# Kernel optimization log

Measured on AMD Instinct MI355X. Metric: run time of the kernel, lower is better.

The kernel has to match this reference:

```python
import jax, jax.numpy as jnp
import numpy as np

Tx, V, D = 512, 100, 64
DM, NH, DFF, NL = 512, 8, 2048, 2
H, DATT, FCH, OUT = 256, 128, 256, 2


def setup_inputs() -> dict:
    key = jax.random.key(0)
    ks = jax.random.split(key, 16)
    s = 0.02
    w = lambda k, shape: jax.random.normal(k, shape, jnp.float32) * s
    return dict(
        x_data=jax.random.normal(ks[0], (1, Tx, V, D), jnp.float32),
        feat_w=w(ks[1], (DM, D)), feat_b=jnp.zeros((DM,), jnp.float32),
        in_w=w(ks[2], (NL, 3 * DM, DM)), in_b=jnp.zeros((NL, 3 * DM), jnp.float32),
        out_w=w(ks[3], (NL, DM, DM)), out_b=jnp.zeros((NL, DM), jnp.float32),
        ff1_w=w(ks[4], (NL, DFF, DM)), ff1_b=jnp.zeros((NL, DFF), jnp.float32),
        ff2_w=w(ks[5], (NL, DM, DFF)), ff2_b=jnp.zeros((NL, DM), jnp.float32),
        ln1_g=jnp.ones((NL, DM), jnp.float32), ln1_b=jnp.zeros((NL, DM), jnp.float32),
        ln2_g=jnp.ones((NL, DM), jnp.float32), ln2_b=jnp.zeros((NL, DM), jnp.float32),
        att1_w=w(ks[6], (DATT, DM + H)), att1_b=jnp.zeros((DATT,), jnp.float32),
        att2_w=w(ks[7], (1, DATT)), att2_b=jnp.zeros((1,), jnp.float32),
        lstm_wih=w(ks[8], (4 * H, DM)), lstm_whh=w(ks[9], (4 * H, H)),
        lstm_bih=jnp.zeros((4 * H,), jnp.float32), lstm_bhh=jnp.zeros((4 * H,), jnp.float32),
        fc1_w=w(ks[10], (FCH, DM + H)), fc1_b=jnp.zeros((FCH,), jnp.float32),
        fc2_w=w(ks[11], (OUT, FCH)), fc2_b=jnp.zeros((OUT,), jnp.float32),
    )


def _layernorm(x, g, b):
    m = x.mean(-1, keepdims=True)
    v = x.var(-1, keepdims=True)
    return (x - m) * jax.lax.rsqrt(v + 1e-5) * g + b


def _forward(x_data, feat_w, feat_b, in_w, in_b, out_w, out_b, ff1_w, ff1_b,
             ff2_w, ff2_b, ln1_g, ln1_b, ln2_g, ln2_b, att1_w, att1_b,
             att2_w, att2_b, lstm_wih, lstm_whh, lstm_bih, lstm_bhh,
             fc1_w, fc1_b, fc2_w, fc2_b):
    x = x_data[0]                              # [Tx, V, D]
    x = jnp.swapaxes(x, 0, 1)                  # [V, Tx, D]  (seq=V, batch=Tx)
    x = x @ feat_w.T + feat_b                  # feature mapping -> [V, Tx, DM]
    # sinusoidal positional encoding over the V (seq) axis
    pos = jnp.arange(V, dtype=jnp.float32)[:, None]
    div = jnp.exp(jnp.arange(0, DM, 2, dtype=jnp.float32) * (-np.log(10000.0) / DM))
    pe = jnp.zeros((V, DM), jnp.float32)
    pe = pe.at[:, 0::2].set(jnp.sin(pos * div)).at[:, 1::2].set(jnp.cos(pos * div))
    x = x + pe[:, None, :]
    hd = DM // NH
    for l in range(NL):                        # post-norm TransformerEncoderLayer
        qkv = x @ in_w[l].T + in_b[l]          # [V, Tx, 3*DM]
        q, k, v = jnp.split(qkv, 3, axis=-1)
        q = q.reshape(V, Tx, NH, hd)
        k = k.reshape(V, Tx, NH, hd)
        v = v.reshape(V, Tx, NH, hd)
        scores = jnp.einsum('ibhd,jbhd->bhij', q, k) / np.sqrt(hd).astype(np.float32)
        attn = jax.nn.softmax(scores, axis=-1)
        ctx = jnp.einsum('bhij,jbhd->ibhd', attn, v).reshape(V, Tx, DM)
        x = _layernorm(x + ctx @ out_w[l].T + out_b[l], ln1_g[l], ln1_b[l])
        ff = jax.nn.relu(x @ ff1_w[l].T + ff1_b[l]) @ ff2_w[l].T + ff2_b[l]
        x = _layernorm(x + ff, ln2_g[l], ln2_b[l])
    hs = jnp.swapaxes(x, 0, 1)                 # [Tx, V, DM]

    def step(carry, h_i):                      # h_i: [V, DM]
        s_h, s_c = carry                       # [1, H] each
        att_in = jnp.concatenate([h_i, jnp.broadcast_to(s_h, (V, H))], axis=1)
        a1 = jnp.tanh(att_in @ att1_w.T + att1_b)
        a2 = a1 @ att2_w.T + att2_b            # [V, 1]
        a2 = a2 - jnp.max(a2)
        alpha = jnp.exp(a2)
        alpha = alpha / (jnp.sum(alpha, axis=0, keepdims=True) + 1e-15)
        c = jnp.sum(alpha * h_i, axis=0, keepdims=True)   # [1, DM]
        gates = c @ lstm_wih.T + lstm_bih + s_h @ lstm_whh.T + lstm_bhh
        i_g, f_g, g_g, o_g = jnp.split(gates, 4, axis=-1)
        s_c_new = jax.nn.sigmoid(f_g) * s_c + jax.nn.sigmoid(i_g) * jnp.tanh(g_g)
        s_h_new = jax.nn.sigmoid(o_g) * jnp.tanh(s_c_new)
        fc_in = jnp.concatenate([c, s_h], axis=1)  # uses PREVIOUS hidden, per original
        fc = jax.nn.relu(fc_in @ fc1_w.T + fc1_b) @ fc2_w.T + fc2_b
        log_prob = jax.nn.log_softmax(fc, axis=1)  # [1, OUT]
        return (s_h_new, s_c_new), log_prob

    init = (jnp.zeros((1, H), jnp.float32), jnp.zeros((1, H), jnp.float32))
    _, logs = jax.lax.scan(step, init, hs)
    return logs[-1]                            # last timestep's log-probs [1, OUT]


def reference(x_data, feat_w, feat_b, in_w, in_b, out_w, out_b, ff1_w, ff1_b,
              ff2_w, ff2_b, ln1_g, ln1_b, ln2_g, ln2_b, att1_w, att1_b,
              att2_w, att2_b, lstm_wih, lstm_whh, lstm_bih, lstm_bhh,
              fc1_w, fc1_b, fc2_w, fc2_b):
    return _forward(x_data, feat_w, feat_b, in_w, in_b, out_w, out_b, ff1_w,
                    ff1_b, ff2_w, ff2_b, ln1_g, ln1_b, ln2_g, ln2_b, att1_w,
                    att1_b, att2_w, att2_b, lstm_wih, lstm_whh, lstm_bih,
                    lstm_bhh, fc1_w, fc1_b, fc2_w, fc2_b)
```

## Files before the change

### kernel.cpp

```cpp
#include <hip/hip_runtime.h>
#include <hip/hip_bf16.h>


typedef __attribute__((ext_vector_type(8))) short short8;
typedef __attribute__((ext_vector_type(4))) float f32x4;

__device__ __forceinline__ int jglob_of(int e0, int jl) { return ((jl >> 4) << 8) + e0 + (jl & 15); }
__device__ __forceinline__ float blo(unsigned u) { return __uint_as_float(u << 16); }
__device__ __forceinline__ float bhi(unsigned u) { return __uint_as_float(u & 0xffff0000u); }
__device__ __forceinline__ short f2bs(float x) {
  union { __hip_bfloat16 h; short s; } u; u.h = __float2bfloat16(x); return u.s;
}
__device__ __forceinline__ float tanhf_fast(float x) {
  float e = __expf(2.f * x);
  return 1.f - 2.f * __builtin_amdgcn_rcpf(e + 1.f);
}

#define GLL16(GSRC, LDST) \
  __builtin_amdgcn_global_load_lds( \
      (const __attribute__((address_space(1))) unsigned int*)(GSRC), \
      (__attribute__((address_space(3))) unsigned int*)(LDST), 16, 0, 0)

__global__ __launch_bounds__(256) void pe_kernel(float* __restrict__ pe) {
  int idx = blockIdx.x * 256 + threadIdx.x;
  if (idx >= 100 * 512) return;
  int v = idx >> 9, n = idx & 511;
  float d = expf(-(float)(n & ~1) * (9.2103403719761836f / 512.0f));
  float ang = (float)v * d;
  pe[idx] = (n & 1) ? cosf(ang) : sinf(ang);
}

__global__ __launch_bounds__(256) void cvt_kernel(const float* __restrict__ src,
                                                  __hip_bfloat16* __restrict__ dst, int n) {
  int i = blockIdx.x * 256 + threadIdx.x;
  if (i < n) dst[i] = __float2bfloat16(src[i]);
}

__global__ __launch_bounds__(256) void gemm_bf16(
    const __hip_bfloat16* __restrict__ A, long aBase, int aDiv, long aSA, long aSB,
    const __hip_bfloat16* __restrict__ W, int ldw,
    const float* __restrict__ bias,
    float* __restrict__ outF, __hip_bfloat16* __restrict__ outB,
    long oBase, int oDiv, long oSA, long oSB,
    int K, int addTo, int relu)
{
  __shared__ __hip_bfloat16 As[128 * 64];
  __shared__ __hip_bfloat16 Bs[128 * 64];
  const int tid = threadIdx.x;
  const int rT = blockIdx.y * 128, nT = blockIdx.x * 128;
  const int wave = tid >> 6, lane = tid & 63;
  const int wr = wave >> 1, wc = wave & 1;
  const int lrow = lane & 15, lkg = lane >> 4;

  long asrc[4], bsrc[4];
  const int sc8 = ((lane & 7) ^ (lane >> 3)) * 8;
#pragma unroll
  for (int i = 0; i < 4; ++i) {
    const int chunk = wave * 4 + i;
    const int row = chunk * 8 + (lane >> 3);
    const int gr = rT + row;
    asrc[i] = aBase + (long)(gr / aDiv) * aSA + (long)(gr % aDiv) * aSB + sc8;
    bsrc[i] = (long)(nT + row) * ldw + sc8;
  }

  f32x4 acc[4][4];
#pragma unroll
  for (int i = 0; i < 4; ++i)
#pragma unroll
    for (int j = 0; j < 4; ++j) acc[i][j] = (f32x4){0.f, 0.f, 0.f, 0.f};

  for (int k0 = 0; k0 < K; k0 += 64) {
#pragma unroll
    for (int i = 0; i < 4; ++i) {
      const int chunk = wave * 4 + i;
      GLL16(A + asrc[i] + k0, &As[chunk * 512]);
      GLL16(W + bsrc[i] + k0, &Bs[chunk * 512]);
    }
    __syncthreads();
#pragma unroll
    for (int ks = 0; ks < 2; ++ks) {
      short8 af[4], bfv[4];
#pragma unroll
      for (int f = 0; f < 4; ++f) {
        const int Ra = wr * 64 + f * 16 + lrow;
        af[f] = *(const short8*)&As[Ra * 64 + (((ks * 4 + lkg) ^ (Ra & 7)) * 8)];
        const int Rb = wc * 64 + f * 16 + lrow;
        bfv[f] = *(const short8*)&Bs[Rb * 64 + (((ks * 4 + lkg) ^ (Rb & 7)) * 8)];
      }
#pragma unroll
      for (int fm = 0; fm < 4; ++fm)
#pragma unroll
        for (int fn = 0; fn < 4; ++fn)
          acc[fm][fn] = __builtin_amdgcn_mfma_f32_16x16x32_bf16(af[fm], bfv[fn], acc[fm][fn], 0, 0, 0);
    }
    __syncthreads();
  }

  float bias_v[4];
#pragma unroll
  for (int fn = 0; fn < 4; ++fn)
    bias_v[fn] = bias ? bias[nT + wc * 64 + fn * 16 + lrow] : 0.f;

#pragma unroll
  for (int fm = 0; fm < 4; ++fm) {
#pragma unroll
    for (int r = 0; r < 4; ++r) {
      const int grow = rT + wr * 64 + fm * 16 + lkg * 4 + r;
      const long obase_r = oBase + (long)(grow / oDiv) * oSA + (long)(grow % oDiv) * oSB;
#pragma unroll
      for (int fn = 0; fn < 4; ++fn) {
        const int gcol = nT + wc * 64 + fn * 16 + lrow;
        float v = acc[fm][fn][r] + bias_v[fn];
        if (relu) v = fmaxf(v, 0.f);
        const long o = obase_r + gcol;
        if (outF) { if (addTo) v += outF[o]; outF[o] = v; }
        else outB[o] = __float2bfloat16(v);
      }
    }
  }
}

__global__ __launch_bounds__(256) void gemm_mfma(
    const float* __restrict__ A, long aBase, int aDiv, long aSA, long aSB,
    const float* __restrict__ W, int ldw,
    const float* __restrict__ bias,
    const float* __restrict__ extra, int extraDiv,
    float* __restrict__ outF, __hip_bfloat16* __restrict__ outB,
    __hip_bfloat16* __restrict__ outB2,
    long oBase, int oDiv, long oSA, long oSB, long oSC,
    int N, int K, int addTo, int relu)
{
  __shared__ short As[2][128][40];
  __shared__ short Bs[2][128][40];
  const int tid = threadIdx.x;
  const int rT = blockIdx.y * 128, nT = blockIdx.x * 128;
  const int wave = tid >> 6, lane = tid & 63;
  const int wr = wave >> 1, wc = wave & 1;
  const int lrow = lane & 15, lkg = lane >> 4;
  const int srow = tid >> 1, shf = tid & 1;

  const long arow = aBase + (long)((rT + srow) / aDiv) * aSA + (long)((rT + srow) % aDiv) * aSB + shf * 16;
  const long brow = (long)(nT + srow) * ldw + shf * 16;

  f32x4 acc[4][4];
#pragma unroll
  for (int i = 0; i < 4; ++i)
#pragma unroll
    for (int j = 0; j < 4; ++j) acc[i][j] = (f32x4){0.f, 0.f, 0.f, 0.f};

  float4 ra[4], rb[4];
#define LOADT(K0) do { \
    const float* _pa = A + arow + (K0); \
    ra[0] = *(const float4*)(_pa); ra[1] = *(const float4*)(_pa + 4); \
    ra[2] = *(const float4*)(_pa + 8); ra[3] = *(const float4*)(_pa + 12); \
    const float* _pb = W + brow + (K0); \
    rb[0] = *(const float4*)(_pb); rb[1] = *(const float4*)(_pb + 4); \
    rb[2] = *(const float4*)(_pb + 8); rb[3] = *(const float4*)(_pb + 12); \
  } while (0)

#define CVST(DST, X, Y) do { \
    short8 _v; \
    _v[0] = f2bs((X).x); _v[1] = f2bs((X).y); _v[2] = f2bs((X).z); _v[3] = f2bs((X).w); \
    _v[4] = f2bs((Y).x); _v[5] = f2bs((Y).y); _v[6] = f2bs((Y).z); _v[7] = f2bs((Y).w); \
    *(short8*)(DST) = _v; \
  } while (0)

#define STAGE(BUF) do { \
    CVST(&As[BUF][srow][shf * 16],     ra[0], ra[1]); \
    CVST(&As[BUF][srow][shf * 16 + 8], ra[2], ra[3]); \
    CVST(&Bs[BUF][srow][shf * 16],     rb[0], rb[1]); \
    CVST(&Bs[BUF][srow][shf * 16 + 8], rb[2], rb[3]); \
  } while (0)

  LOADT(0);
  STAGE(0);
  __syncthreads();

  int cur = 0;
  for (int k0 = 0; k0 < K; k0 += 32) {
    const bool nlast = (k0 + 32 < K);
    if (nlast) LOADT(k0 + 32);
    short8 af[4], bfv[4];
#pragma unroll
    for (int f = 0; f < 4; ++f)
      af[f] = *(const short8*)&As[cur][wr * 64 + f * 16 + lrow][lkg * 8];
#pragma unroll
    for (int f = 0; f < 4; ++f)
      bfv[f] = *(const short8*)&Bs[cur][wc * 64 + f * 16 + lrow][lkg * 8];
#pragma unroll
    for (int fm = 0; fm < 4; ++fm)
#pragma unroll
      for (int fn = 0; fn < 4; ++fn)
        acc[fm][fn] = __builtin_amdgcn_mfma_f32_16x16x32_bf16(af[fm], bfv[fn], acc[fm][fn], 0, 0, 0);
    if (nlast) STAGE(cur ^ 1);
    __syncthreads();
    cur ^= 1;
  }

  float bias_v[4];
#pragma unroll
  for (int fn = 0; fn < 4; ++fn)
    bias_v[fn] = bias ? bias[nT + wc * 64 + fn * 16 + lrow] : 0.f;

#pragma unroll
  for (int fm = 0; fm < 4; ++fm) {
#pragma unroll
    for (int r = 0; r < 4; ++r) {
      const int grow = rT + wr * 64 + fm * 16 + lkg * 4 + r;
      const long obase_r = oBase + (long)(grow / oDiv) * oSA + (long)(grow % oDiv) * oSB;
      const long exrow = (long)(grow / extraDiv) * N;
#pragma unroll
      for (int fn = 0; fn < 4; ++fn) {
        const int gcol = nT + wc * 64 + fn * 16 + lrow;
        float v = acc[fm][fn][r] + bias_v[fn];
        if (extra) v += extra[exrow + gcol];
        if (relu) v = fmaxf(v, 0.f);
        const long o = obase_r + (long)gcol * oSC;
        if (outF) { if (addTo) v += outF[o]; outF[o] = v; }
        else outB[o] = __float2bfloat16(v);
        if (outB2) outB2[o] = __float2bfloat16(v);
      }
    }
  }
#undef LOADT
#undef CVST
#undef STAGE
}

__global__ __launch_bounds__(256) void attn_kernel(
    const __hip_bfloat16* __restrict__ qkv, __hip_bfloat16* __restrict__ outY)
{
  __shared__ float q_s[100][68];
  __shared__ float k_s[100][68];
  __shared__ float v_s[100][68];
  __shared__ float S_s[100][104];
  __shared__ float rs_s[100];
  const int h = blockIdx.x, bl = blockIdx.y, tid = threadIdx.x;

  for (int idx = tid; idx < 100 * 64; idx += 256) {
    int vv = idx >> 6, d = idx & 63;
    long base = ((long)(vv * 128 + bl)) * 1536 + h * 64 + d;
    q_s[vv][d] = __bfloat162float(qkv[base]);
    k_s[vv][d] = __bfloat162float(qkv[base + 512]);
    v_s[vv][d] = __bfloat162float(qkv[base + 1024]);
  }
  __syncthreads();

  const int ty = tid >> 4, tx = tid & 15;
  for (int i0 = 0; i0 < 128; i0 += 64) {
    for (int j0 = 0; j0 < 128; j0 += 64) {
      float acc[4][4];
#pragma unroll
      for (int r = 0; r < 4; ++r)
#pragma unroll
        for (int c = 0; c < 4; ++c) acc[r][c] = 0.f;
      for (int d = 0; d < 64; d += 4) {
        float4 qv[4], kv[4];
#pragma unroll
        for (int r = 0; r < 4; ++r) {
          int ii = i0 + ty * 4 + r; ii = (ii < 100) ? ii : 99;
          qv[r] = *(const float4*)&q_s[ii][d];
        }
#pragma unroll
        for (int c = 0; c < 4; ++c) {
          int jj = j0 + tx * 4 + c; jj = (jj < 100) ? jj : 99;
          kv[c] = *(const float4*)&k_s[jj][d];
        }
#pragma unroll
        for (int r = 0; r < 4; ++r)
#pragma unroll
          for (int c = 0; c < 4; ++c)
            acc[r][c] += qv[r].x * kv[c].x + qv[r].y * kv[c].y + qv[r].z * kv[c].z + qv[r].w * kv[c].w;
      }
#pragma unroll
      for (int r = 0; r < 4; ++r)
#pragma unroll
        for (int c = 0; c < 4; ++c) {
          int ii = i0 + ty * 4 + r, jj = j0 + tx * 4 + c;
          if (ii < 100 && jj < 100) S_s[ii][jj] = acc[r][c] * 0.125f;
        }
    }
  }
  __syncthreads();
  if (tid < 100) {
    float m = -1e30f;
    for (int j = 0; j < 100; ++j) m = fmaxf(m, S_s[tid][j]);
    float s = 0.f;
    for (int j = 0; j < 100; ++j) { float e = __expf(S_s[tid][j] - m); S_s[tid][j] = e; s += e; }
    rs_s[tid] = 1.f / s;
  }
  __syncthreads();
  for (int i0 = 0; i0 < 128; i0 += 64) {
    float acc[4][4];
#pragma unroll
    for (int r = 0; r < 4; ++r)
#pragma unroll
      for (int c = 0; c < 4; ++c) acc[r][c] = 0.f;
    for (int j = 0; j < 100; ++j) {
      float av[4];
#pragma unroll
      for (int r = 0; r < 4; ++r) {
        int ii = i0 + ty * 4 + r; ii = (ii < 100) ? ii : 99;
        av[r] = S_s[ii][j];
      }
      const float4 vv4 = *(const float4*)&v_s[j][tx * 4];
#pragma unroll
      for (int r = 0; r < 4; ++r) {
        acc[r][0] += av[r] * vv4.x; acc[r][1] += av[r] * vv4.y;
        acc[r][2] += av[r] * vv4.z; acc[r][3] += av[r] * vv4.w;
      }
    }
#pragma unroll
    for (int r = 0; r < 4; ++r) {
      int ii = i0 + ty * 4 + r;
      if (ii < 100) {
        float inv = rs_s[ii];
        __hip_bfloat16* op = outY + ((long)ii * 128 + bl) * 512 + h * 64 + tx * 4;
        op[0] = __float2bfloat16(acc[r][0] * inv);
        op[1] = __float2bfloat16(acc[r][1] * inv);
        op[2] = __float2bfloat16(acc[r][2] * inv);
        op[3] = __float2bfloat16(acc[r][3] * inv);
      }
    }
  }
}

__global__ __launch_bounds__(256) void ln_kernel(float* __restrict__ X,
    __hip_bfloat16* __restrict__ Xb,
    const float* __restrict__ g, const float* __restrict__ b)
{
  const int row = blockIdx.x * 4 + (threadIdx.x >> 6);
  const int lane = threadIdx.x & 63;
  float* x = X + (long)row * 512;
  __hip_bfloat16* xb = Xb + (long)row * 512;
  float v[8]; float s = 0.f, sq = 0.f;
#pragma unroll
  for (int i = 0; i < 8; ++i) { v[i] = x[lane + i * 64]; s += v[i]; sq += v[i] * v[i]; }
#pragma unroll
  for (int off = 32; off; off >>= 1) { s += __shfl_xor(s, off, 64); sq += __shfl_xor(sq, off, 64); }
  const float mean = s * (1.f / 512.f);
  const float var = sq * (1.f / 512.f) - mean * mean;
  const float inv = rsqrtf(var + 1e-5f);
#pragma unroll
  for (int i = 0; i < 8; ++i) {
    int c = lane + i * 64;
    float r = (v[i] - mean) * inv * g[c] + b[c];
    x[c] = r;
    xb[c] = __float2bfloat16(r);
  }
}

__global__ void init_kernel(unsigned long long* sh_units, float* c_g) {
  int t = threadIdx.x;
  sh_units[t] = 0ULL;
  sh_units[256 + t] = 0ULL;
  c_g[t] = 0.f; c_g[256 + t] = 0.f;
}

#define DEC_NB 16

__global__ __launch_bounds__(256, 1) void decoder_kernel(
    const float* __restrict__ X,
    const __hip_bfloat16* __restrict__ Pb,
    const __hip_bfloat16* __restrict__ Gb,
    const float* __restrict__ att1_w, const float* __restrict__ att1_b,
    const float* __restrict__ att2_w,
    const float* __restrict__ whh,
    const float* __restrict__ bih, const float* __restrict__ bhh,
    const float* __restrict__ fc1_w, const float* __restrict__ fc1_b,
    const float* __restrict__ fc2_w, const float* __restrict__ fc2_b,
    unsigned long long* sh_units,
    float* c_g,
    float* __restrict__ out)
{
  if (blockIdx.x & 7) return;
  const int tid = threadIdx.x;
  const int blk = blockIdx.x >> 3;
  const int e0 = blk * 16;

  __shared__ __align__(16) float Whh_s[64][260];
  __shared__ __align__(16) unsigned short W1b_s[128][264];
  __shared__ __align__(16) float s_h_s[256];
  __shared__ float w2_s[128], ub_s[128], bsum_s[64];
  __shared__ float u_s[128], sc_s[16];
  __shared__ float a2_s[104];
  __shared__ float red_s[256];
  __shared__ float gates_s[64];
  __shared__ float red4_s[4];
  __shared__ float fcin_s[768];
  __shared__ float fca_s[256];

  for (int idx = tid; idx < 64 * 256; idx += 256) {
    int jl = idx >> 8, k = idx & 255;
    Whh_s[jl][k] = whh[(long)jglob_of(e0, jl) * 256 + k];
  }
  for (int idx = tid; idx < 128 * 256; idx += 256) {
    int j = idx >> 8, k = idx & 255;
    union { __hip_bfloat16 h; unsigned short u; } cv;
    cv.h = __float2bfloat16(att1_w[(long)j * 768 + 512 + k]);
    W1b_s[j][k] = cv.u;
  }
  if (tid < 128) { w2_s[tid] = att2_w[tid]; ub_s[tid] = att1_b[tid]; }
  if (tid < 64) {
    int jg = jglob_of(e0, tid);
    bsum_s[tid] = bih[jg] + bhh[jg];
  }
  if (tid < 16) sc_s[tid] = 0.f;
  if (tid < 4) a2_s[100 + tid] = 0.f;

  const int pv = tid >> 1, ppart = tid & 1;
  const int pvv = (pv < 100) ? pv : 99;
  const int gjl = tid >> 2, gq = tid & 3;
  const long gRowOff = (long)jglob_of(e0, gjl) * 100 + gq * 26;

  unsigned PCa[32], PCb[32];
  unsigned GCa[13], GCb[13];

#define PREFETCH(T1, PCd, GCd) do { \
    const uint4* _pp = (const uint4*)Pb + ((((long)(T1) * 100 + pvv) * 128 + ppart * 64) >> 3); \
    _Pragma("unroll") \
    for (int _i = 0; _i < 8; ++_i) { \
      uint4 _t = _pp[_i]; \
      (PCd)[4*_i] = _t.x; (PCd)[4*_i+1] = _t.y; (PCd)[4*_i+2] = _t.z; (PCd)[4*_i+3] = _t.w; \
    } \
    const unsigned* _gp = (const unsigned*)(Gb + (long)(T1) * 102400 + gRowOff); \
    _Pragma("unroll") \
    for (int _i = 0; _i < 13; ++_i) (GCd)[_i] = _gp[_i]; \
  } while (0)

#define STEP(T, PCc, GCc, PCn, GCn) do { \
     \
    { \
      unsigned long long* _up = &sh_units[((((T) & 1) ^ 1) << 8) + tid]; \
      unsigned long long _v = __hip_atomic_load(_up, __ATOMIC_RELAXED, __HIP_MEMORY_SCOPE_AGENT); \
      while ((unsigned)(_v >> 32) < (unsigned)(T)) { \
        __builtin_amdgcn_s_sleep(1); \
        _v = __hip_atomic_load(_up, __ATOMIC_RELAXED, __HIP_MEMORY_SCOPE_AGENT); \
      } \
      s_h_s[tid] = __uint_as_float((unsigned)_v); \
    } \
    __syncthreads(); \
     \
    if ((T) + 1 < 512) PREFETCH((T) + 1, PCn, GCn); \
     \
    { const int _j = tid >> 1, _hf = tid & 1; \
      const unsigned short* _wrow = &W1b_s[_j][_hf * 128]; \
      const float* _sh = &s_h_s[_hf * 128]; \
      float _a = 0.f; \
      _Pragma("unroll") \
      for (int _i = 0; _i < 16; ++_i) { \
        uint4 _wv = *(const uint4*)(_wrow + 8 * _i); \
        const float4 _s0 = *(const float4*)(_sh + 8 * _i); \
        const float4 _s1 = *(const float4*)(_sh + 8 * _i + 4); \
        _a += blo(_wv.x) * _s0.x + bhi(_wv.x) * _s0.y + blo(_wv.y) * _s0.z + bhi(_wv.y) * _s0.w \
            + blo(_wv.z) * _s1.x + bhi(_wv.z) * _s1.y + blo(_wv.w) * _s1.z + bhi(_wv.w) * _s1.w; \
      } \
      _a += __shfl_xor(_a, 1, 64); \
      if (_hf == 0) u_s[_j] = _a + ub_s[_j]; \
    } \
    float _hhv; \
    { const float* _wr = &Whh_s[gjl][gq * 64]; \
      const float* _sh = &s_h_s[gq * 64]; \
      float _a = 0.f; \
      _Pragma("unroll") \
      for (int _i = 0; _i < 16; ++_i) { \
        const float4 _w4 = *(const float4*)(_wr + 4 * _i); \
        const float4 _s4 = *(const float4*)(_sh + 4 * _i); \
        _a += _w4.x * _s4.x + _w4.y * _s4.y + _w4.z * _s4.z + _w4.w * _s4.w; \
      } \
      _a += __shfl_xor(_a, 1, 64); \
      _a += __shfl_xor(_a, 2, 64); \
      _hhv = _a; \
    } \
    __syncthreads(); \
     \
    { float _val = 0.f; \
      _Pragma("unroll") \
      for (int _jj = 0; _jj < 64; ++_jj) { \
        unsigned _u = (PCc)[_jj >> 1]; \
        float _pf = (_jj & 1) ? bhi(_u) : blo(_u); \
        int _col = ppart * 64 + _jj; \
        _val += tanhf_fast(_pf + u_s[_col]) * w2_s[_col]; \
      } \
      _val += __shfl_xor(_val, 1, 64); \
      if (ppart == 0 && pv < 100) a2_s[pv] = _val; \
    } \
    __syncthreads(); \
     \
    if (tid < 64) { \
      float _x0 = a2_s[tid]; \
      float _x1 = (tid + 64 < 100) ? a2_s[tid + 64] : -3.0e38f; \
      float _m = fmaxf(_x0, _x1); \
      _Pragma("unroll") \
      for (int _o = 32; _o; _o >>= 1) _m = fmaxf(_m, __shfl_xor(_m, _o, 64)); \
      float _e0 = __expf(_x0 - _m); \
      float _e1 = (tid + 64 < 100) ? __expf(_x1 - _m) : 0.f; \
      float _s = _e0 + _e1; \
      _Pragma("unroll") \
      for (int _o = 32; _o; _o >>= 1) _s += __shfl_xor(_s, _o, 64); \
      const float _inv = 1.f / (_s + 1e-15f); \
      a2_s[tid] = _e0 * _inv; \
      if (tid + 64 < 100) a2_s[tid + 64] = _e1 * _inv; \
    } \
    __syncthreads(); \
     \
    { float _p = 0.f; \
      _Pragma("unroll") \
      for (int _i = 0; _i < 13; ++_i) { \
        unsigned _u = (GCc)[_i]; \
        _p += a2_s[gq * 26 + 2 * _i] * blo(_u); \
        _p += a2_s[gq * 26 + 2 * _i + 1] * bhi(_u); \
      } \
      _p += __shfl_xor(_p, 1, 64); \
      _p += __shfl_xor(_p, 2, 64); \
      if (gq == 0) gates_s[gjl] = _p + _hhv + bsum_s[gjl]; \
    } \
    __syncthreads(); \
     \
    if ((T) < 511) { \
      if (tid < 16) { \
        const float _ig = gates_s[tid], _fg = gates_s[16 + tid]; \
        const float _gg = gates_s[32 + tid], _og = gates_s[48 + tid]; \
        const float _si = 1.f / (1.f + __expf(-_ig)); \
        const float _sf = 1.f / (1.f + __expf(-_fg)); \
        const float _so = 1.f / (1.f + __expf(-_og)); \
        const float _sc = _sf * sc_s[tid] + _si * tanhf(_gg); \
        sc_s[tid] = _sc; \
        const float _sh2 = _so * tanhf(_sc); \
        const unsigned long long _v = \
            ((unsigned long long)(unsigned)((T) + 1) << 32) | (unsigned long long)__float_as_uint(_sh2); \
        __hip_atomic_store(&sh_units[(((T) & 1) << 8) + e0 + tid], _v, \
                           __ATOMIC_RELAXED, __HIP_MEMORY_SCOPE_AGENT); \
      } \
    } else { \
      const int _dl = tid & 31, _vs = tid >> 5; \
      const int _v0 = _vs * 13, _v1 = (_v0 + 13 < 100) ? _v0 + 13 : 100; \
      float _ac = 0.f; \
      for (int _v = _v0; _v < _v1; ++_v) \
        _ac += a2_s[_v] * X[((long)(_v * 512 + 511)) * 512 + blk * 32 + _dl]; \
      red_s[tid] = _ac; \
      __syncthreads(); \
      if (tid < 32) { \
        float _cc = 0.f; \
        _Pragma("unroll") \
        for (int _s = 0; _s < 8; ++_s) _cc += red_s[_s * 32 + tid]; \
        __hip_atomic_store(&c_g[blk * 32 + tid], _cc, __ATOMIC_RELAXED, __HIP_MEMORY_SCOPE_AGENT); \
      } \
      __syncthreads(); \
      if (tid == 0) \
        __hip_atomic_store(&sh_units[256 + e0], 512ULL << 32, \
                           __ATOMIC_RELEASE, __HIP_MEMORY_SCOPE_AGENT); \
    } \
  } while (0)

  PREFETCH(0, PCa, GCa);
  __syncthreads();

  for (int t2 = 0; t2 < 512; t2 += 2) {
    STEP(t2,     PCa, GCa, PCb, GCb);
    STEP(t2 + 1, PCb, GCb, PCa, GCa);
  }

  if (blk == 0) {
    if (tid < DEC_NB) {
      while ((unsigned)(__hip_atomic_load(&sh_units[256 + tid * 16],
                 __ATOMIC_RELAXED, __HIP_MEMORY_SCOPE_AGENT) >> 32) < 512u)
        __builtin_amdgcn_s_sleep(1);
    }
    __builtin_amdgcn_fence(__ATOMIC_ACQUIRE, "agent");
    __syncthreads();
    fcin_s[tid]       = __hip_atomic_load(&c_g[tid],       __ATOMIC_RELAXED, __HIP_MEMORY_SCOPE_AGENT);
    fcin_s[256 + tid] = __hip_atomic_load(&c_g[256 + tid], __ATOMIC_RELAXED, __HIP_MEMORY_SCOPE_AGENT);
    fcin_s[512 + tid] = s_h_s[tid];
    __syncthreads();
    float acc = fc1_b[tid];
    const float* w = fc1_w + (long)tid * 768;
    for (int k = 0; k < 768; ++k) acc += w[k] * fcin_s[k];
    fca_s[tid] = fmaxf(acc, 0.f);
    __syncthreads();
    if (tid < 128) {
      const int r = tid >> 6, k0 = tid & 63;
      float a = 0.f;
#pragma unroll
      for (int s = 0; s < 4; ++s) a += fc2_w[r * 256 + k0 + s * 64] * fca_s[k0 + s * 64];
#pragma unroll
      for (int off = 32; off; off >>= 1) a += __shfl_xor(a, off, 64);
      if (k0 == 0) red4_s[r] = a + fc2_b[r];
    }
    __syncthreads();
    if (tid == 0) {
      const float l0 = red4_s[0], l1 = red4_s[1];
      const float m = fmaxf(l0, l1);
      const float ls = logf(__expf(l0 - m) + __expf(l1 - m));
      out[0] = l0 - m - ls;
      out[1] = l1 - m - ls;
    }
  }
#undef PREFETCH
#undef STEP
}

extern "C" void kernel_launch(void* const* d_in, const int* in_sizes, int n_in,
                              void* d_out, int out_size, void* d_ws, size_t ws_size,
                              hipStream_t stream) {
  const float* x_data  = (const float*)d_in[0];
  const float* feat_w  = (const float*)d_in[1];
  const float* feat_b  = (const float*)d_in[2];
  const float* in_w    = (const float*)d_in[3];
  const float* in_b    = (const float*)d_in[4];
  const float* out_w   = (const float*)d_in[5];
  const float* out_b   = (const float*)d_in[6];
  const float* ff1_w   = (const float*)d_in[7];
  const float* ff1_b   = (const float*)d_in[8];
  const float* ff2_w   = (const float*)d_in[9];
  const float* ff2_b   = (const float*)d_in[10];
  const float* ln1_g   = (const float*)d_in[11];
  const float* ln1_b   = (const float*)d_in[12];
  const float* ln2_g   = (const float*)d_in[13];
  const float* ln2_b   = (const float*)d_in[14];
  const float* att1_w  = (const float*)d_in[15];
  const float* att1_b  = (const float*)d_in[16];
  const float* att2_w  = (const float*)d_in[17];
  const float* lstm_wih = (const float*)d_in[19];
  const float* lstm_whh = (const float*)d_in[20];
  const float* lstm_bih = (const float*)d_in[21];
  const float* lstm_bhh = (const float*)d_in[22];
  const float* fc1_w   = (const float*)d_in[23];
  const float* fc1_b   = (const float*)d_in[24];
  const float* fc2_w   = (const float*)d_in[25];
  const float* fc2_b   = (const float*)d_in[26];

  float* ws   = (float*)d_ws;
  float* Xf   = ws;
  float* R    = Xf + 26214400;
  __hip_bfloat16* Xb   = (__hip_bfloat16*)R;
  __hip_bfloat16* qkvb = (__hip_bfloat16*)(R + 13107200);
  __hip_bfloat16* ctxb = (__hip_bfloat16*)(R + 22937600);
  __hip_bfloat16* ffh  = (__hip_bfloat16*)(R + 13107200);
  __hip_bfloat16* wb   = (__hip_bfloat16*)(R + 26214400);
  __hip_bfloat16* in_wb  = wb;
  __hip_bfloat16* out_wb = wb + 1572864;
  __hip_bfloat16* ff1_wb = out_wb + 524288;
  __hip_bfloat16* ff2_wb = ff1_wb + 2097152;
  __hip_bfloat16* PbB = (__hip_bfloat16*)R;
  __hip_bfloat16* GbB = (__hip_bfloat16*)(R + 3276800);
  float* pe    = R + 29491200;
  unsigned long long* sh_units = (unsigned long long*)(pe + 51200);
  float* c_g   = (float*)(sh_units + 512);

  pe_kernel<<<200, 256, 0, stream>>>(pe);
  cvt_kernel<<<(1572864 + 255) / 256, 256, 0, stream>>>(in_w, in_wb, 1572864);
  cvt_kernel<<<(524288 + 255) / 256, 256, 0, stream>>>(out_w, out_wb, 524288);
  cvt_kernel<<<(2097152 + 255) / 256, 256, 0, stream>>>(ff1_w, ff1_wb, 2097152);
  cvt_kernel<<<(2097152 + 255) / 256, 256, 0, stream>>>(ff2_w, ff2_wb, 2097152);

  gemm_mfma<<<dim3(4, 400), 256, 0, stream>>>(
      x_data, 0L, 512, 64L, 6400L, feat_w, 64, feat_b, pe, 512,
      Xf, nullptr, Xb, 0L, 1 << 30, 0L, 512L, 1L, 512, 64, 0, 0);

  for (int l = 0; l < 2; ++l) {
    for (int c = 0; c < 4; ++c) {
      const long b0 = c * 128;
      gemm_bf16<<<dim3(12, 100), 256, 0, stream>>>(
          Xb, b0 * 512, 128, 262144L, 512L,
          in_wb + (long)l * 786432, 512, in_b + l * 1536,
          nullptr, qkvb, 0L, 1 << 30, 0L, 1536L, 512, 0, 0);
      attn_kernel<<<dim3(8, 128), 256, 0, stream>>>(qkvb, ctxb);
      gemm_bf16<<<dim3(4, 100), 256, 0, stream>>>(
          ctxb, 0L, 1 << 30, 0L, 512L,
          out_wb + (long)l * 262144, 512, out_b + l * 512,
          Xf, nullptr, b0 * 512, 128, 262144L, 512L, 512, 1, 0);
    }
    ln_kernel<<<12800, 256, 0, stream>>>(Xf, Xb, ln1_g + l * 512, ln1_b + l * 512);
    for (int rc = 0; rc < 4; ++rc) {
      const long r0 = (long)rc * 12800;
      gemm_bf16<<<dim3(16, 100), 256, 0, stream>>>(
          Xb, r0 * 512, 1 << 30, 0L, 512L,
          ff1_wb + (long)l * 1048576, 512, ff1_b + l * 2048,
          nullptr, ffh, 0L, 1 << 30, 0L, 2048L, 512, 0, 1);
      gemm_bf16<<<dim3(4, 100), 256, 0, stream>>>(
          ffh, 0L, 1 << 30, 0L, 2048L,
          ff2_wb + (long)l * 1048576, 2048, ff2_b + l * 512,
          Xf, nullptr, r0 * 512, 1 << 30, 0L, 512L, 2048, 1, 0);
    }
    ln_kernel<<<12800, 256, 0, stream>>>(Xf, Xb, ln2_g + l * 512, ln2_b + l * 512);
  }

  gemm_mfma<<<dim3(1, 400), 256, 0, stream>>>(
      Xf, 0L, 100, 512L, 262144L, att1_w, 768, nullptr, nullptr, 1,
      nullptr, PbB, nullptr, 0L, 1 << 30, 0L, 128L, 1L, 128, 512, 0, 0);
  gemm_mfma<<<dim3(8, 400), 256, 0, stream>>>(
      Xf, 0L, 100, 512L, 262144L, lstm_wih, 512, nullptr, nullptr, 1,
      nullptr, GbB, nullptr, 0L, 100, 102400L, 1L, 100L, 1024, 512, 0, 0);

  init_kernel<<<1, 256, 0, stream>>>(sh_units, c_g);
  decoder_kernel<<<DEC_NB * 8, 256, 0, stream>>>(
      Xf, PbB, GbB, att1_w, att1_b, att2_w,
      lstm_whh, lstm_bih, lstm_bhh, fc1_w, fc1_b, fc2_w, fc2_b,
      sh_units, c_g, (float*)d_out);
}
```

Measured before the change: 5.723 ms.

## Compute attention QK^T and PV with bf16 MFMA instead of scalar FP32

Rewrites the attention kernel to keep Q, K and a transposed V as bf16 in shared memory, zero-padded to 112/128 rows. Both matmuls now run on 16x16x32 bf16 MFMA tiles instead of FP32 scalar FMA loops. Softmax is split across two threads per row and writes unnormalised probabilities as bf16 for the PV MFMA. The goal is to remove the FP32 ALU cost of attention. The trade-offs are a ~100KB shared arena that limits occupancy, and extra rounding from storing probabilities in bf16.

```diff
diff --git a/kernel.cpp b/kernel.cpp
--- a/kernel.cpp
+++ b/kernel.cpp
@@ -230,96 +230,90 @@
 __global__ __launch_bounds__(256) void attn_kernel(
     const __hip_bfloat16* __restrict__ qkv, __hip_bfloat16* __restrict__ outY)
 {
-  __shared__ float q_s[100][68];
-  __shared__ float k_s[100][68];
-  __shared__ float v_s[100][68];
-  __shared__ float S_s[100][104];
-  __shared__ float rs_s[100];
+  __shared__ __align__(16) char arena[101632];
+  unsigned short* Qs = (unsigned short*)arena;
+  unsigned short* Ks = Qs + 8064;
+  unsigned short* Vt = Ks + 8064;
+  float* S = (float*)(arena + 49664);
+  unsigned short* Sb = (unsigned short*)arena;
+  __shared__ float rs_s[112];
+
   const int h = blockIdx.x, bl = blockIdx.y, tid = threadIdx.x;
-
-  for (int idx = tid; idx < 100 * 64; idx += 256) {
-    int vv = idx >> 6, d = idx & 63;
-    long base = ((long)(vv * 128 + bl)) * 1536 + h * 64 + d;
-    q_s[vv][d] = __bfloat162float(qkv[base]);
-    k_s[vv][d] = __bfloat162float(qkv[base + 512]);
-    v_s[vv][d] = __bfloat162float(qkv[base + 1024]);
+  const unsigned short* q16 = (const unsigned short*)qkv;
+
+  for (int idx = tid; idx < 6400; idx += 256) {
+    int v = idx >> 6, d = idx & 63;
+    long base = ((long)(v * 128 + bl)) * 1536 + h * 64 + d;
+    Qs[v * 72 + d] = q16[base];
+    Ks[v * 72 + d] = q16[base + 512];
+    Vt[d * 136 + v] = q16[base + 1024];
+  }
+  for (int idx = tid; idx < 12 * 64; idx += 256) {
+    int r = 100 + (idx >> 6), c = idx & 63;
+    Qs[r * 72 + c] = 0; Ks[r * 72 + c] = 0;
+  }
+  for (int idx = tid; idx < 64 * 36; idx += 256) {
+    int d = idx / 36, c = 100 + idx % 36;
+    Vt[d * 136 + c] = 0;
   }
   __syncthreads();
 
-  const int ty = tid >> 4, tx = tid & 15;
-  for (int i0 = 0; i0 < 128; i0 += 64) {
-    for (int j0 = 0; j0 < 128; j0 += 64) {
-      float acc[4][4];
-#pragma unroll
-      for (int r = 0; r < 4; ++r)
-#pragma unroll
-        for (int c = 0; c < 4; ++c) acc[r][c] = 0.f;
-      for (int d = 0; d < 64; d += 4) {
-        float4 qv[4], kv[4];
-#pragma unroll
-        for (int r = 0; r < 4; ++r) {
-          int ii = i0 + ty * 4 + r; ii = (ii < 100) ? ii : 99;
-          qv[r] = *(const float4*)&q_s[ii][d];
-        }
-#pragma unroll
-        for (int c = 0; c < 4; ++c) {
-          int jj = j0 + tx * 4 + c; jj = (jj < 100) ? jj : 99;
-          kv[c] = *(const float4*)&k_s[jj][d];
-        }
-#pragma unroll
-        for (int r = 0; r < 4; ++r)
-#pragma unroll
-          for (int c = 0; c < 4; ++c)
-            acc[r][c] += qv[r].x * kv[c].x + qv[r].y * kv[c].y + qv[r].z * kv[c].z + qv[r].w * kv[c].w;
-      }
-#pragma unroll
-      for (int r = 0; r < 4; ++r)
-#pragma unroll
-        for (int c = 0; c < 4; ++c) {
-          int ii = i0 + ty * 4 + r, jj = j0 + tx * 4 + c;
-          if (ii < 100 && jj < 100) S_s[ii][jj] = acc[r][c] * 0.125f;
-        }
-    }
+  const int wave = tid >> 6, lane = tid & 63;
+  const int lrow = lane & 15, lkg = lane >> 4;
+
+  for (int tt = wave; tt < 49; tt += 4) {
+    const int tm = tt / 7, tn = tt % 7;
+    f32x4 a = (f32x4){0.f, 0.f, 0.f, 0.f};
+#pragma unroll
+    for (int ks = 0; ks < 2; ++ks) {
+      short8 af = *(const short8*)&Qs[(tm * 16 + lrow) * 72 + ks * 32 + lkg * 8];
+      short8 bf = *(const short8*)&Ks[(tn * 16 + lrow) * 72 + ks * 32 + lkg * 8];
+      a = __builtin_amdgcn_mfma_f32_16x16x32_bf16(af, bf, a, 0, 0, 0);
+    }
+#pragma unroll
+    for (int r = 0; r < 4; ++r)
+      S[(tm * 16 + lkg * 4 + r) * 116 + tn * 16 + lrow] = a[r] * 0.125f;
   }
   __syncthreads();
-  if (tid < 100) {
-    float m = -1e30f;
-    for (int j = 0; j < 100; ++j) m = fmaxf(m, S_s[tid][j]);
+
+  {
+    unsigned* p = (unsigned*)Sb;
+    for (int idx = tid; idx < 7616; idx += 256) p[idx] = 0;
+  }
+  __syncthreads();
+
+  if (tid < 200) {
+    const int r = tid >> 1, hf = tid & 1;
+    const float* srow = S + r * 116 + hf * 50;
+    float m = -3.0e38f;
+    for (int c = 0; c < 50; ++c) m = fmaxf(m, srow[c]);
+    m = fmaxf(m, __shfl_xor(m, 1, 64));
     float s = 0.f;
-    for (int j = 0; j < 100; ++j) { float e = __expf(S_s[tid][j] - m); S_s[tid][j] = e; s += e; }
-    rs_s[tid] = 1.f / s;
+    for (int c = 0; c < 50; ++c) {
+      float e = __expf(srow[c] - m);
+      Sb[r * 136 + hf * 50 + c] = (unsigned short)f2bs(e);
+      s += e;
+    }
+    s += __shfl_xor(s, 1, 64);
+    if (hf == 0) rs_s[r] = 1.f / s;
   }
   __syncthreads();
-  for (int i0 = 0; i0 < 128; i0 += 64) {
-    float acc[4][4];
-#pragma unroll
-    for (int r = 0; r < 4; ++r)
-#pragma unroll
-      for (int c = 0; c < 4; ++c) acc[r][c] = 0.f;
-    for (int j = 0; j < 100; ++j) {
-      float av[4];
-#pragma unroll
-      for (int r = 0; r < 4; ++r) {
-        int ii = i0 + ty * 4 + r; ii = (ii < 100) ? ii : 99;
-        av[r] = S_s[ii][j];
-      }
-      const float4 vv4 = *(const float4*)&v_s[j][tx * 4];
-#pragma unroll
-      for (int r = 0; r < 4; ++r) {
-        acc[r][0] += av[r] * vv4.x; acc[r][1] += av[r] * vv4.y;
-        acc[r][2] += av[r] * vv4.z; acc[r][3] += av[r] * vv4.w;
-      }
+
+  for (int tt = wave; tt < 28; tt += 4) {
+    const int tm = tt >> 2, tn = tt & 3;
+    f32x4 a = (f32x4){0.f, 0.f, 0.f, 0.f};
+#pragma unroll
+    for (int kc = 0; kc < 4; ++kc) {
+      short8 af = *(const short8*)&Sb[(tm * 16 + lrow) * 136 + kc * 32 + lkg * 8];
+      short8 bf = *(const short8*)&Vt[(tn * 16 + lrow) * 136 + kc * 32 + lkg * 8];
+      a = __builtin_amdgcn_mfma_f32_16x16x32_bf16(af, bf, a, 0, 0, 0);
     }
 #pragma unroll
     for (int r = 0; r < 4; ++r) {
-      int ii = i0 + ty * 4 + r;
-      if (ii < 100) {
-        float inv = rs_s[ii];
-        __hip_bfloat16* op = outY + ((long)ii * 128 + bl) * 512 + h * 64 + tx * 4;
-        op[0] = __float2bfloat16(acc[r][0] * inv);
-        op[1] = __float2bfloat16(acc[r][1] * inv);
-        op[2] = __float2bfloat16(acc[r][2] * inv);
-        op[3] = __float2bfloat16(acc[r][3] * inv);
+      const int m = tm * 16 + lkg * 4 + r;
+      if (m < 100) {
+        const int n = tn * 16 + lrow;
+        outY[((long)m * 128 + bl) * 512 + h * 64 + n] = __float2bfloat16(a[r] * rs_s[m]);
       }
     }
   }
```

Measured after the change: 5.276 ms. -7.8%, faster.
